# Optimization experiments

Measured on AMD Instinct MI355X. Metric: run time of the kernel, lower is better.

## Reference

```python
import jax, jax.numpy as jnp
import numpy as np

EPS_NORM = 1e-12  # F.normalize eps
EPS_LN = 1e-5     # nn.LayerNorm eps


def setup_inputs() -> dict:
    key = jax.random.key(0)
    ks = jax.random.split(key, 8)
    B, T, N, D = 16, 12, 300, 64
    feat = jax.random.normal(ks[0], (B, T, N, D), dtype=jnp.float32)
    weights = jax.random.uniform(ks[1], (D,), dtype=jnp.float32)
    sc = 1.0 / np.sqrt(D)
    w1 = jax.random.normal(ks[2], (D, D), dtype=jnp.float32) * sc
    b1 = jax.random.normal(ks[3], (D,), dtype=jnp.float32) * sc
    w2 = jax.random.normal(ks[4], (D, D), dtype=jnp.float32) * sc
    b2 = jax.random.normal(ks[5], (D,), dtype=jnp.float32) * sc
    gamma = jnp.ones((D,), dtype=jnp.float32)
    beta = jnp.zeros((D,), dtype=jnp.float32)
    return {"feat": feat, "weights": weights, "w1": w1, "b1": b1,
            "w2": w2, "b2": b2, "gamma": gamma, "beta": beta}


def _windows(x, T2):
    # x: [B,T,N,D] -> [B,T2,3N,D] where window i = concat(x[:,i], x[:,i+1], x[:,i+2]) over node dim
    B, T, N, D = x.shape
    w = jnp.stack([x[:, i:i + T2] for i in range(3)], axis=2)  # [B,T2,3,N,D]
    return w.reshape(B, T2, 3 * N, D)


def reference(feat, weights, w1, b1, w2, b2, gamma, beta):
    B, T, N, D = feat.shape
    T2 = T - 2
    # learned edge gating + L2-normalize along feature dim
    wf = feat * jax.nn.sigmoid(weights)
    nrm = jnp.sqrt(jnp.sum(wf * wf, axis=-1, keepdims=True))
    wf = wf / jnp.maximum(nrm, EPS_NORM)
    win = _windows(feat, T2)   # [B,T2,3N,D]
    wwin = _windows(wf, T2)    # [B,T2,3N,D]
    # learned adjacency: cosine-similarity gram matrix per window
    adj = jnp.einsum('btnd,btmd->btnm', wwin, wwin)  # [B,T2,3N,3N]
    # norm_adj: row normalization, zero rows stay zero
    deg = jnp.sum(adj, axis=-1, keepdims=True)
    dinv = jnp.where(deg == 0, 0.0, 1.0 / jnp.where(deg == 0, 1.0, deg))
    adj = adj * dinv
    # aggregate, keep last N rows (current timestep nodes)
    agg = jnp.einsum('btnm,btmd->btnd', adj, win)[:, :, -N:, :]  # [B,T2,N,D]
    # FFN (dropout is eval-mode identity): Linear -> ReLU -> Linear
    h = jnp.maximum(agg @ w1 + b1, 0.0) @ w2 + b2
    # residual + LayerNorm
    s = feat[:, 2:] + h
    mu = jnp.mean(s, axis=-1, keepdims=True)
    var = jnp.mean((s - mu) ** 2, axis=-1, keepdims=True)
    out = (s - mu) * jax.lax.rsqrt(var + EPS_LN) * gamma + beta
    return out  # [B, T-2, N, D]
```

## Files before the change

kernel.cpp:

```cpp
#include <hip/hip_runtime.h>
#include <math.h>

#define BB  16
#define TT  12
#define T2C 10
#define NN  300
#define DD  64
#define M3  900
#define NW  (BB*T2C)

typedef _Float16 f16;
typedef __attribute__((ext_vector_type(8)))  _Float16 f16x8;
typedef __attribute__((ext_vector_type(16))) float    f32x16;

#define KS 72

static __device__ inline unsigned pk2(f16 a, f16 b) {
    union { f16 h[2]; unsigned u; } x; x.h[0] = a; x.h[1] = b; return x.u;
}

__global__ __launch_bounds__(256) void k_pm(const float* __restrict__ feat,
                                            const float* __restrict__ weights,
                                            const float* __restrict__ w1,
                                            const float* __restrict__ w2,
                                            float* __restrict__ sigw,
                                            float* __restrict__ invn,
                                            float* __restrict__ tsum,
                                            f16* __restrict__ w1f,
                                            f16* __restrict__ w2f,
                                            float* __restrict__ Mt) {
    int blk = blockIdx.x;
    int tid = threadIdx.x;

    if (blk == BB * TT) {
        if (tid < 64) sigw[tid] = 1.0f / (1.0f + expf(-weights[tid]));
        for (int p = tid; p < 1024; p += 256) {
            int lane = p & 63, s = p >> 6;
            int mat = s >> 3, loc = s & 7, ct = loc >> 2, ks = loc & 3;
            int hcol = ct * 32 + (lane & 31);
            const float* w = mat ? w2 : w1;
            f16* dst = (mat ? w2f : w1f) + ((size_t)loc * 64 + lane) * 8;
            f16x8 v;
            #pragma unroll
            for (int j = 0; j < 8; j++) {
                int d = ks * 16 + 8 * (lane >> 5) + j;
                v[j] = (f16)w[d * DD + hcol];
            }
            *(f16x8*)dst = v;
        }
        return;
    }

    __shared__ f16 Kti[64 * KS];
    __shared__ f16 Vtt[64 * KS];
    __shared__ float sspart[64][8];
    __shared__ float invrow[64];
    __shared__ float tspp[32][64];

    int bt = blk;
    int row0 = bt * NN;
    int wv = tid >> 6, lane = tid & 63;
    int l31 = lane & 31, lh = lane >> 5;
    int ci = wv & 1, di = wv >> 1;
    int mr = (tid & 31) * 2;
    int cb = (tid >> 5) * 8;

    float sg[8];
    {
        float4 wv0 = *(const float4*)(weights + cb);
        float4 wv1 = *(const float4*)(weights + cb + 4);
        sg[0] = 1.f/(1.f+expf(-wv0.x)); sg[1] = 1.f/(1.f+expf(-wv0.y));
        sg[2] = 1.f/(1.f+expf(-wv0.z)); sg[3] = 1.f/(1.f+expf(-wv0.w));
        sg[4] = 1.f/(1.f+expf(-wv1.x)); sg[5] = 1.f/(1.f+expf(-wv1.y));
        sg[6] = 1.f/(1.f+expf(-wv1.z)); sg[7] = 1.f/(1.f+expf(-wv1.w));
    }

    float tacc[8];
    #pragma unroll
    for (int i = 0; i < 8; i++) tacc[i] = 0.f;
    f32x16 acc;
    #pragma unroll
    for (int i = 0; i < 16; i++) acc[i] = 0.f;

    for (int ep = 0; ep < 5; ep++) {
        __syncthreads();
        int gm0 = ep * 64 + mr, gm1 = gm0 + 1;
        bool ok0 = gm0 < NN, ok1 = gm1 < NN;
        int g0 = row0 + (ok0 ? gm0 : 0);
        int g1 = row0 + (ok1 ? gm1 : 0);
        float4 a0 = *(const float4*)(feat + (size_t)g0 * DD + cb);
        float4 a1 = *(const float4*)(feat + (size_t)g0 * DD + cb + 4);
        float4 b0 = *(const float4*)(feat + (size_t)g1 * DD + cb);
        float4 b1 = *(const float4*)(feat + (size_t)g1 * DD + cb + 4);
        float av[8] = {a0.x, a0.y, a0.z, a0.w, a1.x, a1.y, a1.z, a1.w};
        float bv[8] = {b0.x, b0.y, b0.z, b0.w, b1.x, b1.y, b1.z, b1.w};

        float ss0 = 0.f, ss1 = 0.f;
        #pragma unroll
        for (int i = 0; i < 8; i++) {
            float xa = av[i] * sg[i], xb = bv[i] * sg[i];
            ss0 += xa * xa; ss1 += xb * xb;
        }
        sspart[mr][tid >> 5] = ss0;
        sspart[mr + 1][tid >> 5] = ss1;
        __syncthreads();
        if (tid < 64) {
            float s = sspart[tid][0] + sspart[tid][1] + sspart[tid][2] + sspart[tid][3]
                    + sspart[tid][4] + sspart[tid][5] + sspart[tid][6] + sspart[tid][7];
            float in = 1.0f / fmaxf(sqrtf(s), 1e-12f);
            invrow[tid] = in;
            int grow = ep * 64 + tid;
            if (grow < NN) invn[row0 + grow] = in;
        }
        __syncthreads();
        float i0 = ok0 ? invrow[mr] : 0.f;
        float i1 = ok1 ? invrow[mr + 1] : 0.f;
        #pragma unroll
        for (int i = 0; i < 8; i++) {
            *(unsigned*)&Kti[(cb + i) * KS + mr] = pk2((f16)(av[i] * i0), (f16)(bv[i] * i1));
            *(unsigned*)&Vtt[(cb + i) * KS + mr] = pk2((f16)av[i], (f16)bv[i]);
            tacc[i] += av[i] * i0 + bv[i] * i1;
        }
        __syncthreads();
        #pragma unroll
        for (int ks = 0; ks < 4; ks++) {
            f16x8 af = *(const f16x8*)&Kti[(ci * 32 + l31) * KS + ks * 16 + 8 * lh];
            f16x8 bf = *(const f16x8*)&Vtt[(di * 32 + l31) * KS + ks * 16 + 8 * lh];
            acc = __builtin_amdgcn_mfma_f32_32x32x16_f16(af, bf, acc, 0, 0, 0);
        }
    }

    float* mb = Mt + (size_t)bt * 4096;
    #pragma unroll
    for (int g = 0; g < 4; g++)
        *(float4*)&mb[(di * 32 + l31) * 64 + ci * 32 + 8 * g + 4 * lh] =
            make_float4(acc[4 * g + 0], acc[4 * g + 1], acc[4 * g + 2], acc[4 * g + 3]);

    #pragma unroll
    for (int i = 0; i < 8; i++) tspp[tid & 31][cb + i] = tacc[i] * sg[i];
    __syncthreads();
    if (tid < 64) {
        float s = 0.f;
        #pragma unroll
        for (int g = 0; g < 32; g++) s += tspp[g][tid];
        tsum[(size_t)bt * 64 + tid] = s;
    }
}

__global__ __launch_bounds__(256) void k_U(const float* __restrict__ feat,
                                           const float* __restrict__ sigw,
                                           const float* __restrict__ invn,
                                           const float* __restrict__ tsum,
                                           const float* __restrict__ Mt,
                                           const f16* __restrict__ w1f,
                                           const f16* __restrict__ w2f,
                                           const float* __restrict__ b1,
                                           const float* __restrict__ b2,
                                           const float* __restrict__ gamma,
                                           const float* __restrict__ beta,
                                           float* __restrict__ out) {
    __shared__ union __align__(16) {
        f16 Mh[64 * KS];
        f16 Hl[64 * KS];
    } MH;
    __shared__ float Ol[64 * 68];
    __shared__ float red[64][4][2];
    __shared__ float rmax[64][4];
    __shared__ float scls[64];
    __shared__ float isls[64];
    __shared__ float degp[64][4];
    __shared__ float degs[64];
    __shared__ float ksumL[64];

    int blk = blockIdx.x;
    int wdw = blk % NW;
    int rb  = blk / NW;
    int t2 = wdw % T2C, b = wdw / T2C;
    int n0 = rb * 64;
    int qrow0 = (b * TT + t2 + 2) * NN;
    int tid = threadIdx.x;
    int wv = tid >> 6, lane = tid & 63;
    int l31 = lane & 31, lh = lane >> 5;
    int nt = wv & 1;
    int dt = wv >> 1;
    int ct = wv & 1, rt = wv >> 1;
    int r = tid >> 2, q = tid & 3, c0 = q * 16;

    f16x8 w1a[4], w2a[4];
    #pragma unroll
    for (int ks = 0; ks < 4; ks++) {
        w1a[ks] = *(const f16x8*)(w1f + ((size_t)(ct * 4 + ks) * 64 + lane) * 8);
        w2a[ks] = *(const f16x8*)(w2f + ((size_t)(ct * 4 + ks) * 64 + lane) * 8);
    }

    if (tid < 64) {
        const float* tp = tsum + (size_t)(b * TT + t2) * 64 + tid;
        ksumL[tid] = tp[0] + tp[64] + tp[128];
    }

    f16x8 qf[4];
    {
        int nloc = n0 + nt * 32 + l31;
        bool ok = nloc < NN;
        int gr = qrow0 + (ok ? nloc : 0);
        float in = ok ? invn[gr] : 0.f;
        #pragma unroll
        for (int ks = 0; ks < 4; ks++) {
            int cc = ks * 16 + 8 * lh;
            float4 f0 = *(const float4*)(feat + (size_t)gr * DD + cc);
            float4 f1 = *(const float4*)(feat + (size_t)gr * DD + cc + 4);
            float4 s0 = *(const float4*)(sigw + cc);
            float4 s1 = *(const float4*)(sigw + cc + 4);
            f16x8 qv;
            qv[0] = (f16)(f0.x * s0.x * s0.x * in); qv[1] = (f16)(f0.y * s0.y * s0.y * in);
            qv[2] = (f16)(f0.z * s0.z * s0.z * in); qv[3] = (f16)(f0.w * s0.w * s0.w * in);
            qv[4] = (f16)(f1.x * s1.x * s1.x * in); qv[5] = (f16)(f1.y * s1.y * s1.y * in);
            qv[6] = (f16)(f1.z * s1.z * s1.z * in); qv[7] = (f16)(f1.w * s1.w * s1.w * in);
            qf[ks] = qv;
        }
    }

    float ms[16];
    {
        const float* mtb = Mt + (size_t)(b * TT + t2) * 4096 + r * 64 + c0;
        #pragma unroll
        for (int i = 0; i < 4; i++) {
            float4 m0 = *(const float4*)(mtb + 4 * i);
            float4 m1 = *(const float4*)(mtb + 4096 + 4 * i);
            float4 m2 = *(const float4*)(mtb + 8192 + 4 * i);
            ms[4*i+0] = m0.x + m1.x + m2.x; ms[4*i+1] = m0.y + m1.y + m2.y;
            ms[4*i+2] = m0.z + m1.z + m2.z; ms[4*i+3] = m0.w + m1.w + m2.w;
        }
    }

    int n = n0 + r;
    int nc = (n < NN) ? n : (NN - 1);
    size_t frow = ((size_t)qrow0 + nc) * DD;
    float fv[16];
    #pragma unroll
    for (int i = 0; i < 4; i++) {
        float4 f = *(const float4*)(feat + frow + c0 + 4 * i);
        fv[4*i+0] = f.x; fv[4*i+1] = f.y; fv[4*i+2] = f.z; fv[4*i+3] = f.w;
    }
    float invq = invn[qrow0 + nc];

    __syncthreads();

    {
        float p = 0.f;
        #pragma unroll
        for (int i = 0; i < 4; i++) {
            float4 s = *(const float4*)(sigw + c0 + 4 * i);
            float4 k = *(const float4*)(ksumL + c0 + 4 * i);
            p += fv[4*i+0] * s.x * k.x + fv[4*i+1] * s.y * k.y
               + fv[4*i+2] * s.z * k.z + fv[4*i+3] * s.w * k.w;
        }
        degp[r][q] = p * invq;
    }

    #pragma unroll
    for (int hhalf = 0; hhalf < 2; hhalf++) {
        f16x8 v;
        #pragma unroll
        for (int j = 0; j < 8; j++) v[j] = (f16)ms[8 * hhalf + j];
        *(f16x8*)&MH.Mh[r * KS + c0 + 8 * hhalf] = v;
    }
    __syncthreads();

    if (tid < 64)
        degs[tid] = degp[tid][0] + degp[tid][1] + degp[tid][2] + degp[tid][3];

    f32x16 ua;
    #pragma unroll
    for (int i = 0; i < 16; i++) ua[i] = 0.f;
    #pragma unroll
    for (int ks = 0; ks < 4; ks++) {
        f16x8 af = *(const f16x8*)&MH.Mh[(dt * 32 + l31) * KS + ks * 16 + 8 * lh];
        ua = __builtin_amdgcn_mfma_f32_32x32x16_f16(af, qf[ks], ua, 0, 0, 0);
    }
    __syncthreads();

    {
        int nl = nt * 32 + l31;
        float dg = degs[nl];
        float dinv = (dg == 0.f) ? 0.f : 1.f / dg;
        #pragma unroll
        for (int g = 0; g < 4; g++)
            *(float4*)&Ol[nl * 68 + dt * 32 + 8 * g + 4 * lh] =
                make_float4(ua[4*g+0] * dinv, ua[4*g+1] * dinv,
                            ua[4*g+2] * dinv, ua[4*g+3] * dinv);
    }
    __syncthreads();

    {
        float mx = 0.f;
        #pragma unroll
        for (int i = 0; i < 16; i += 4) {
            float4 f = *(const float4*)&Ol[r * 68 + c0 + i];
            mx = fmaxf(mx, fmaxf(fmaxf(fabsf(f.x), fabsf(f.y)),
                                 fmaxf(fabsf(f.z), fabsf(f.w))));
        }
        rmax[r][q] = mx;
    }
    __syncthreads();
    if (q == 0) {
        float rm = fmaxf(fmaxf(rmax[r][0], rmax[r][1]),
                         fmaxf(rmax[r][2], rmax[r][3]));
        int e = 0;
        frexpf(rm, &e);
        scls[r] = (rm > 1.f) ? exp2f((float)-e) : 1.f;
        isls[r] = (rm > 1.f) ? exp2f((float)e) : 1.f;
    }
    __syncthreads();

    float sclrow = scls[rt * 32 + l31];
    f32x16 hc;
    #pragma unroll
    for (int i = 0; i < 16; i++) hc[i] = 0.f;
    #pragma unroll
    for (int ks = 0; ks < 4; ks++) {
        const float* prw = &Ol[(rt * 32 + l31) * 68 + ks * 16 + 8 * lh];
        float4 pa = *(const float4*)prw;
        float4 pb = *(const float4*)(prw + 4);
        f16x8 bf;
        bf[0] = (f16)(pa.x * sclrow); bf[1] = (f16)(pa.y * sclrow);
        bf[2] = (f16)(pa.z * sclrow); bf[3] = (f16)(pa.w * sclrow);
        bf[4] = (f16)(pb.x * sclrow); bf[5] = (f16)(pb.y * sclrow);
        bf[6] = (f16)(pb.z * sclrow); bf[7] = (f16)(pb.w * sclrow);
        hc = __builtin_amdgcn_mfma_f32_32x32x16_f16(w1a[ks], bf, hc, 0, 0, 0);
    }
    #pragma unroll
    for (int g = 0; g < 4; g++) {
        union { f16 h[4]; uint2 u; } p;
        #pragma unroll
        for (int i = 0; i < 4; i++) {
            int hcol = ct * 32 + 8 * g + 4 * lh + i;
            p.h[i] = (f16)fmaxf(hc[4 * g + i] + sclrow * b1[hcol], 0.f);
        }
        *(uint2*)&MH.Hl[(rt * 32 + l31) * KS + ct * 32 + 8 * g + 4 * lh] = p.u;
    }
    __syncthreads();

    f32x16 oc;
    #pragma unroll
    for (int i = 0; i < 16; i++) oc[i] = 0.f;
    #pragma unroll
    for (int ks = 0; ks < 4; ks++) {
        f16x8 bf = *(const f16x8*)&MH.Hl[(rt * 32 + l31) * KS + ks * 16 + 8 * lh];
        oc = __builtin_amdgcn_mfma_f32_32x32x16_f16(w2a[ks], bf, oc, 0, 0, 0);
    }
    __syncthreads();
    #pragma unroll
    for (int g = 0; g < 4; g++) {
        float4 o4 = make_float4(oc[4*g+0], oc[4*g+1], oc[4*g+2], oc[4*g+3]);
        *(float4*)&Ol[(rt * 32 + l31) * 68 + ct * 32 + 8 * g + 4 * lh] = o4;
    }
    __syncthreads();

    float is = isls[r];
    float v[16];
    float sum = 0.f;
    #pragma unroll
    for (int i = 0; i < 16; i++) {
        int c = c0 + i;
        float x = Ol[r * 68 + c] * is + b2[c] + fv[i];
        v[i] = x; sum += x;
    }
    red[r][q][0] = sum;
    __syncthreads();
    float mu = (red[r][0][0] + red[r][1][0] + red[r][2][0] + red[r][3][0]) * (1.f / 64.f);
    float s2 = 0.f;
    #pragma unroll
    for (int i = 0; i < 16; i++) { float d = v[i] - mu; s2 += d * d; }
    red[r][q][1] = s2;
    __syncthreads();
    float var = (red[r][0][1] + red[r][1][1] + red[r][2][1] + red[r][3][1]) * (1.f / 64.f);
    float rs = rsqrtf(var + 1e-5f);
    if (n < NN) {
        size_t grow = (size_t)wdw * NN + n;
        #pragma unroll
        for (int i4 = 0; i4 < 4; i4++) {
            int c = c0 + 4 * i4;
            float4 g4 = *(const float4*)(gamma + c);
            float4 be = *(const float4*)(beta + c);
            float4 o4;
            o4.x = (v[4*i4+0] - mu) * rs * g4.x + be.x;
            o4.y = (v[4*i4+1] - mu) * rs * g4.y + be.y;
            o4.z = (v[4*i4+2] - mu) * rs * g4.z + be.z;
            o4.w = (v[4*i4+3] - mu) * rs * g4.w + be.w;
            *(float4*)(out + grow * DD + c) = o4;
        }
    }
}

extern "C" void kernel_launch(void* const* d_in, const int* in_sizes, int n_in,
                              void* d_out, int out_size, void* d_ws, size_t ws_size,
                              hipStream_t stream) {
    const float* feat    = (const float*)d_in[0];
    const float* weights = (const float*)d_in[1];
    const float* w1      = (const float*)d_in[2];
    const float* b1      = (const float*)d_in[3];
    const float* w2      = (const float*)d_in[4];
    const float* b2      = (const float*)d_in[5];
    const float* gamma   = (const float*)d_in[6];
    const float* beta    = (const float*)d_in[7];
    float* out = (float*)d_out;

    float* sigw = (float*)d_ws;
    float* invn = sigw + 64;
    float* tsum = invn + BB * TT * NN;
    f16*   w1f  = (f16*)(tsum + BB * TT * DD);
    f16*   w2f  = w1f + 4096;
    float* Mt   = (float*)(w2f + 4096);

    k_pm<<<BB * TT + 1, 256, 0, stream>>>(feat, weights, w1, w2, sigw, invn,
                                          tsum, w1f, w2f, Mt);
    k_U<<<NW * 5, 256, 0, stream>>>(feat, sigw, invn, tsum, Mt, w1f, w2f,
                                    b1, b2, gamma, beta, out);
}
```

Before: 103.4 us.

## Fuse per-timestep prepass and per-window update into one kernel per window

Replaces the two-kernel scheme with a single kernel that runs one 512-thread block per window. Each block recomputes the 64x64 K^T V summary over all 900 window rows, splitting the reduction across two wave halves, and keeps the inverse norms and key sums in shared memory instead of going through global workspace. It then processes the five 64-row output tiles in two groups. This removes a launch and the global round-trip of the intermediates, and adds software prefetch of feat rows. In exchange, only 160 blocks are launched and each timestep's work is recomputed up to three times across overlapping windows.

```diff
diff --git a/kernel.cpp b/kernel.cpp
--- a/kernel.cpp
+++ b/kernel.cpp
@@ -6,64 +6,63 @@
 #define T2C 10
 #define NN  300
 #define DD  64
-#define M3  900
-#define NW  (BB*T2C)
+#define NWD (BB*T2C)
 
 typedef _Float16 f16;
 typedef __attribute__((ext_vector_type(8)))  _Float16 f16x8;
 typedef __attribute__((ext_vector_type(16))) float    f32x16;
 
-#define KS 72
+#define KSM 136
+#define KS  72
 
 static __device__ inline unsigned pk2(f16 a, f16 b) {
     union { f16 h[2]; unsigned u; } x; x.h[0] = a; x.h[1] = b; return x.u;
 }
 
-__global__ __launch_bounds__(256) void k_pm(const float* __restrict__ feat,
-                                            const float* __restrict__ weights,
-                                            const float* __restrict__ w1,
-                                            const float* __restrict__ w2,
-                                            float* __restrict__ sigw,
-                                            float* __restrict__ invn,
-                                            float* __restrict__ tsum,
-                                            f16* __restrict__ w1f,
-                                            f16* __restrict__ w2f,
-                                            float* __restrict__ Mt) {
+struct P1 {
+    f16 Kti[64 * KSM];
+    f16 Vtt[64 * KSM];
+    float sspart[128][8];
+    float invrow[128];
+};
+struct P2 {
+    float Ol[2][64 * 68];
+    f16   Hl[2][64 * KS];
+    float red[2][64][4][2];
+    float rmax[2][64][4];
+    float scls[2][64];
+    float isls[2][64];
+    float degp[2][64][4];
+    float degs[2][64];
+};
+
+__global__ __launch_bounds__(512, 2) void k_fused(
+        const float* __restrict__ feat,
+        const float* __restrict__ weights,
+        const float* __restrict__ w1,
+        const float* __restrict__ b1,
+        const float* __restrict__ w2,
+        const float* __restrict__ b2,
+        const float* __restrict__ gamma,
+        const float* __restrict__ beta,
+        float* __restrict__ out) {
+    __shared__ union __align__(16) { P1 p1; P2 p2; } SH;
+    __shared__ __align__(16) f16 Mh[64 * KS];
+    __shared__ __align__(16) float invq[NN + 4];
+    __shared__ __align__(16) float ksumL[64];
+    __shared__ __align__(16) float sigwL[64];
+
     int blk = blockIdx.x;
+    int wdw = (blk & 7) * (NWD / 8) + (blk >> 3);
+    int t2 = wdw % T2C, b = wdw / T2C;
     int tid = threadIdx.x;
-
-    if (blk == BB * TT) {
-        if (tid < 64) sigw[tid] = 1.0f / (1.0f + expf(-weights[tid]));
-        for (int p = tid; p < 1024; p += 256) {
-            int lane = p & 63, s = p >> 6;
-            int mat = s >> 3, loc = s & 7, ct = loc >> 2, ks = loc & 3;
-            int hcol = ct * 32 + (lane & 31);
-            const float* w = mat ? w2 : w1;
-            f16* dst = (mat ? w2f : w1f) + ((size_t)loc * 64 + lane) * 8;
-            f16x8 v;
-            #pragma unroll
-            for (int j = 0; j < 8; j++) {
-                int d = ks * 16 + 8 * (lane >> 5) + j;
-                v[j] = (f16)w[d * DD + hcol];
-            }
-            *(f16x8*)dst = v;
-        }
-        return;
-    }
-
-    __shared__ f16 Kti[64 * KS];
-    __shared__ f16 Vtt[64 * KS];
-    __shared__ float sspart[64][8];
-    __shared__ float invrow[64];
-    __shared__ float tspp[32][64];
-
-    int bt = blk;
-    int row0 = bt * NN;
-    int wv = tid >> 6, lane = tid & 63;
-    int l31 = lane & 31, lh = lane >> 5;
-    int ci = wv & 1, di = wv >> 1;
-    int mr = (tid & 31) * 2;
-    int cb = (tid >> 5) * 8;
+    int lane = tid & 63, l31 = lane & 31, lh = lane >> 5;
+    int wv = tid >> 6;
+    int ci = wv & 1, di = (wv >> 1) & 1, kh = wv >> 2;
+    int mr = (tid & 63) * 2;
+    int cb = (tid >> 6) * 8;
+
+    if (tid < 64) sigwL[tid] = 1.0f / (1.0f + expf(-weights[tid]));
 
     float sg[8];
     {
@@ -75,6 +74,8 @@
         sg[6] = 1.f/(1.f+expf(-wv1.z)); sg[7] = 1.f/(1.f+expf(-wv1.w));
     }
 
+    int baserow = (b * TT + t2) * NN;
+
     float tacc[8];
     #pragma unroll
     for (int i = 0; i < 8; i++) tacc[i] = 0.f;
@@ -82,313 +83,308 @@
     #pragma unroll
     for (int i = 0; i < 16; i++) acc[i] = 0.f;
 
-    for (int ep = 0; ep < 5; ep++) {
-        __syncthreads();
-        int gm0 = ep * 64 + mr, gm1 = gm0 + 1;
-        bool ok0 = gm0 < NN, ok1 = gm1 < NN;
-        int g0 = row0 + (ok0 ? gm0 : 0);
-        int g1 = row0 + (ok1 ? gm1 : 0);
-        float4 a0 = *(const float4*)(feat + (size_t)g0 * DD + cb);
-        float4 a1 = *(const float4*)(feat + (size_t)g0 * DD + cb + 4);
-        float4 b0 = *(const float4*)(feat + (size_t)g1 * DD + cb);
-        float4 b1 = *(const float4*)(feat + (size_t)g1 * DD + cb + 4);
-        float av[8] = {a0.x, a0.y, a0.z, a0.w, a1.x, a1.y, a1.z, a1.w};
-        float bv[8] = {b0.x, b0.y, b0.z, b0.w, b1.x, b1.y, b1.z, b1.w};
+#define LOADEP(EP, A, B) do { \
+        int M0_ = (EP) * 128 + mr; \
+        int g0_ = baserow + ((M0_ < 900) ? M0_ : 0); \
+        int g1_ = baserow + ((M0_ + 1 < 900) ? (M0_ + 1) : 0); \
+        float4 a0_ = *(const float4*)(feat + (size_t)g0_ * DD + cb); \
+        float4 a1_ = *(const float4*)(feat + (size_t)g0_ * DD + cb + 4); \
+        float4 b0_ = *(const float4*)(feat + (size_t)g1_ * DD + cb); \
+        float4 b1_ = *(const float4*)(feat + (size_t)g1_ * DD + cb + 4); \
+        A[0]=a0_.x; A[1]=a0_.y; A[2]=a0_.z; A[3]=a0_.w; \
+        A[4]=a1_.x; A[5]=a1_.y; A[6]=a1_.z; A[7]=a1_.w; \
+        B[0]=b0_.x; B[1]=b0_.y; B[2]=b0_.z; B[3]=b0_.w; \
+        B[4]=b1_.x; B[5]=b1_.y; B[6]=b1_.z; B[7]=b1_.w; \
+    } while (0)
+
+    float a_cur[8], b_cur[8];
+    LOADEP(0, a_cur, b_cur);
+
+    #pragma unroll
+    for (int ep = 0; ep < 8; ep++) {
+        int M0 = ep * 128 + mr;
+        bool ok0 = M0 < 900, ok1 = (M0 + 1) < 900;
 
         float ss0 = 0.f, ss1 = 0.f;
         #pragma unroll
         for (int i = 0; i < 8; i++) {
-            float xa = av[i] * sg[i], xb = bv[i] * sg[i];
+            float xa = a_cur[i] * sg[i], xb = b_cur[i] * sg[i];
             ss0 += xa * xa; ss1 += xb * xb;
         }
-        sspart[mr][tid >> 5] = ss0;
-        sspart[mr + 1][tid >> 5] = ss1;
-        __syncthreads();
-        if (tid < 64) {
-            float s = sspart[tid][0] + sspart[tid][1] + sspart[tid][2] + sspart[tid][3]
-                    + sspart[tid][4] + sspart[tid][5] + sspart[tid][6] + sspart[tid][7];
+        SH.p1.sspart[mr][wv] = ss0;
+        SH.p1.sspart[mr + 1][wv] = ss1;
+
+        float a_nxt[8], b_nxt[8];
+        if (ep < 7) LOADEP(ep + 1, a_nxt, b_nxt);
+
+        __syncthreads();
+        if (tid < 128) {
+            float s = SH.p1.sspart[tid][0] + SH.p1.sspart[tid][1]
+                    + SH.p1.sspart[tid][2] + SH.p1.sspart[tid][3]
+                    + SH.p1.sspart[tid][4] + SH.p1.sspart[tid][5]
+                    + SH.p1.sspart[tid][6] + SH.p1.sspart[tid][7];
             float in = 1.0f / fmaxf(sqrtf(s), 1e-12f);
-            invrow[tid] = in;
-            int grow = ep * 64 + tid;
-            if (grow < NN) invn[row0 + grow] = in;
-        }
-        __syncthreads();
-        float i0 = ok0 ? invrow[mr] : 0.f;
-        float i1 = ok1 ? invrow[mr + 1] : 0.f;
+            SH.p1.invrow[tid] = in;
+            int M = ep * 128 + tid;
+            if (M >= 600 && M < 900) invq[M - 600] = in;
+        }
+        __syncthreads();
+        float i0 = ok0 ? SH.p1.invrow[mr] : 0.f;
+        float i1 = ok1 ? SH.p1.invrow[mr + 1] : 0.f;
         #pragma unroll
         for (int i = 0; i < 8; i++) {
-            *(unsigned*)&Kti[(cb + i) * KS + mr] = pk2((f16)(av[i] * i0), (f16)(bv[i] * i1));
-            *(unsigned*)&Vtt[(cb + i) * KS + mr] = pk2((f16)av[i], (f16)bv[i]);
-            tacc[i] += av[i] * i0 + bv[i] * i1;
+            *(unsigned*)&SH.p1.Kti[(cb + i) * KSM + mr] =
+                pk2((f16)(a_cur[i] * i0), (f16)(b_cur[i] * i1));
+            *(unsigned*)&SH.p1.Vtt[(cb + i) * KSM + mr] =
+                pk2((f16)a_cur[i], (f16)b_cur[i]);
+            tacc[i] += a_cur[i] * i0 + b_cur[i] * i1;
         }
         __syncthreads();
         #pragma unroll
         for (int ks = 0; ks < 4; ks++) {
-            f16x8 af = *(const f16x8*)&Kti[(ci * 32 + l31) * KS + ks * 16 + 8 * lh];
-            f16x8 bf = *(const f16x8*)&Vtt[(di * 32 + l31) * KS + ks * 16 + 8 * lh];
+            f16x8 af = *(const f16x8*)&SH.p1.Kti[(ci*32+l31)*KSM + kh*64 + ks*16 + 8*lh];
+            f16x8 bf = *(const f16x8*)&SH.p1.Vtt[(di*32+l31)*KSM + kh*64 + ks*16 + 8*lh];
             acc = __builtin_amdgcn_mfma_f32_32x32x16_f16(af, bf, acc, 0, 0, 0);
         }
-    }
-
-    float* mb = Mt + (size_t)bt * 4096;
+        if (ep < 7) {
+            #pragma unroll
+            for (int i = 0; i < 8; i++) { a_cur[i] = a_nxt[i]; b_cur[i] = b_nxt[i]; }
+        }
+    }
+#undef LOADEP
+
+    __syncthreads();
+    float* Mw   = (float*)SH.p1.Kti;
+    float* tspp = (float*)SH.p1.Vtt;
+    if (kh == 1) {
+        #pragma unroll
+        for (int g4 = 0; g4 < 4; g4++)
+            *(float4*)&Mw[(di*32+l31)*68 + ci*32 + 8*g4 + 4*lh] =
+                make_float4(acc[4*g4+0], acc[4*g4+1], acc[4*g4+2], acc[4*g4+3]);
+    }
     #pragma unroll
-    for (int g = 0; g < 4; g++)
-        *(float4*)&mb[(di * 32 + l31) * 64 + ci * 32 + 8 * g + 4 * lh] =
-            make_float4(acc[4 * g + 0], acc[4 * g + 1], acc[4 * g + 2], acc[4 * g + 3]);
-
-    #pragma unroll
-    for (int i = 0; i < 8; i++) tspp[tid & 31][cb + i] = tacc[i] * sg[i];
+    for (int i = 0; i < 8; i++) tspp[(tid & 63) * 64 + cb + i] = tacc[i] * sg[i];
     __syncthreads();
+    if (kh == 0) {
+        #pragma unroll
+        for (int g4 = 0; g4 < 4; g4++) {
+            float4 m = *(const float4*)&Mw[(di*32+l31)*68 + ci*32 + 8*g4 + 4*lh];
+            union { f16 h[4]; uint2 u; } p;
+            p.h[0] = (f16)(acc[4*g4+0] + m.x);
+            p.h[1] = (f16)(acc[4*g4+1] + m.y);
+            p.h[2] = (f16)(acc[4*g4+2] + m.z);
+            p.h[3] = (f16)(acc[4*g4+3] + m.w);
+            *(uint2*)&Mh[(di*32+l31)*KS + ci*32 + 8*g4 + 4*lh] = p.u;
+        }
+    }
     if (tid < 64) {
         float s = 0.f;
-        #pragma unroll
-        for (int g = 0; g < 32; g++) s += tspp[g][tid];
-        tsum[(size_t)bt * 64 + tid] = s;
-    }
-}
-
-__global__ __launch_bounds__(256) void k_U(const float* __restrict__ feat,
-                                           const float* __restrict__ sigw,
-                                           const float* __restrict__ invn,
-                                           const float* __restrict__ tsum,
-                                           const float* __restrict__ Mt,
-                                           const f16* __restrict__ w1f,
-                                           const f16* __restrict__ w2f,
-                                           const float* __restrict__ b1,
-                                           const float* __restrict__ b2,
-                                           const float* __restrict__ gamma,
-                                           const float* __restrict__ beta,
-                                           float* __restrict__ out) {
-    __shared__ union __align__(16) {
-        f16 Mh[64 * KS];
-        f16 Hl[64 * KS];
-    } MH;
-    __shared__ float Ol[64 * 68];
-    __shared__ float red[64][4][2];
-    __shared__ float rmax[64][4];
-    __shared__ float scls[64];
-    __shared__ float isls[64];
-    __shared__ float degp[64][4];
-    __shared__ float degs[64];
-    __shared__ float ksumL[64];
-
-    int blk = blockIdx.x;
-    int wdw = blk % NW;
-    int rb  = blk / NW;
-    int t2 = wdw % T2C, b = wdw / T2C;
-    int n0 = rb * 64;
+        #pragma unroll 8
+        for (int j = 0; j < 64; j++) s += tspp[j * 64 + tid];
+        ksumL[tid] = s;
+    }
+    __syncthreads();
+
+    int grp = tid >> 8;
+    int ltid = tid & 255;
+    int wv_l = ltid >> 6;
+    int nt = wv_l & 1, dt = wv_l >> 1;
+    int ct = wv_l & 1, rt = wv_l >> 1;
+    int r = ltid >> 2, q = ltid & 3, c0 = q * 16;
     int qrow0 = (b * TT + t2 + 2) * NN;
-    int tid = threadIdx.x;
-    int wv = tid >> 6, lane = tid & 63;
-    int l31 = lane & 31, lh = lane >> 5;
-    int nt = wv & 1;
-    int dt = wv >> 1;
-    int ct = wv & 1, rt = wv >> 1;
-    int r = tid >> 2, q = tid & 3, c0 = q * 16;
 
     f16x8 w1a[4], w2a[4];
     #pragma unroll
     for (int ks = 0; ks < 4; ks++) {
-        w1a[ks] = *(const f16x8*)(w1f + ((size_t)(ct * 4 + ks) * 64 + lane) * 8);
-        w2a[ks] = *(const f16x8*)(w2f + ((size_t)(ct * 4 + ks) * 64 + lane) * 8);
-    }
-
-    if (tid < 64) {
-        const float* tp = tsum + (size_t)(b * TT + t2) * 64 + tid;
-        ksumL[tid] = tp[0] + tp[64] + tp[128];
-    }
-
-    f16x8 qf[4];
-    {
-        int nloc = n0 + nt * 32 + l31;
-        bool ok = nloc < NN;
-        int gr = qrow0 + (ok ? nloc : 0);
-        float in = ok ? invn[gr] : 0.f;
+        f16x8 v1, v2;
+        #pragma unroll
+        for (int j = 0; j < 8; j++) {
+            int drow = ks * 16 + 8 * lh + j;
+            int hcol = ct * 32 + l31;
+            v1[j] = (f16)w1[drow * DD + hcol];
+            v2[j] = (f16)w2[drow * DD + hcol];
+        }
+        w1a[ks] = v1; w2a[ks] = v2;
+    }
+
+    for (int it = 0; it < 3; it++) {
+        int tile = it * 2 + grp;
+        bool act = tile < 5;
+        int n0 = tile * 64;
+
+        __syncthreads();
+
+        f16x8 qf[4];
+        {
+            int nloc = n0 + nt * 32 + l31;
+            bool ok = act && (nloc < NN);
+            int ni = ok ? nloc : 0;
+            int gr = qrow0 + ni;
+            float in = ok ? invq[ni] : 0.f;
+            #pragma unroll
+            for (int ks = 0; ks < 4; ks++) {
+                int cc = ks * 16 + 8 * lh;
+                float4 f0 = *(const float4*)(feat + (size_t)gr * DD + cc);
+                float4 f1 = *(const float4*)(feat + (size_t)gr * DD + cc + 4);
+                float4 s0 = *(const float4*)&sigwL[cc];
+                float4 s1 = *(const float4*)&sigwL[cc + 4];
+                f16x8 qv;
+                qv[0] = (f16)(f0.x*s0.x*s0.x*in); qv[1] = (f16)(f0.y*s0.y*s0.y*in);
+                qv[2] = (f16)(f0.z*s0.z*s0.z*in); qv[3] = (f16)(f0.w*s0.w*s0.w*in);
+                qv[4] = (f16)(f1.x*s1.x*s1.x*in); qv[5] = (f16)(f1.y*s1.y*s1.y*in);
+                qv[6] = (f16)(f1.z*s1.z*s1.z*in); qv[7] = (f16)(f1.w*s1.w*s1.w*in);
+                qf[ks] = qv;
+            }
+        }
+
+        int n = n0 + r;
+        int nc = (n < NN) ? n : (NN - 1);
+        size_t frow = ((size_t)qrow0 + nc) * DD;
+        float fv[16];
+        #pragma unroll
+        for (int i = 0; i < 4; i++) {
+            float4 f = *(const float4*)(feat + frow + c0 + 4 * i);
+            fv[4*i+0] = f.x; fv[4*i+1] = f.y; fv[4*i+2] = f.z; fv[4*i+3] = f.w;
+        }
+        float invqr = invq[nc];
+
+        {
+            float p = 0.f;
+            #pragma unroll
+            for (int i = 0; i < 4; i++) {
+                float4 s = *(const float4*)&sigwL[c0 + 4 * i];
+                float4 k = *(const float4*)&ksumL[c0 + 4 * i];
+                p += fv[4*i+0]*s.x*k.x + fv[4*i+1]*s.y*k.y
+                   + fv[4*i+2]*s.z*k.z + fv[4*i+3]*s.w*k.w;
+            }
+            SH.p2.degp[grp][r][q] = p * invqr;
+        }
+
+        f32x16 ua;
+        #pragma unroll
+        for (int i = 0; i < 16; i++) ua[i] = 0.f;
         #pragma unroll
         for (int ks = 0; ks < 4; ks++) {
-            int cc = ks * 16 + 8 * lh;
-            float4 f0 = *(const float4*)(feat + (size_t)gr * DD + cc);
-            float4 f1 = *(const float4*)(feat + (size_t)gr * DD + cc + 4);
-            float4 s0 = *(const float4*)(sigw + cc);
-            float4 s1 = *(const float4*)(sigw + cc + 4);
-            f16x8 qv;
-            qv[0] = (f16)(f0.x * s0.x * s0.x * in); qv[1] = (f16)(f0.y * s0.y * s0.y * in);
-            qv[2] = (f16)(f0.z * s0.z * s0.z * in); qv[3] = (f16)(f0.w * s0.w * s0.w * in);
-            qv[4] = (f16)(f1.x * s1.x * s1.x * in); qv[5] = (f16)(f1.y * s1.y * s1.y * in);
-            qv[6] = (f16)(f1.z * s1.z * s1.z * in); qv[7] = (f16)(f1.w * s1.w * s1.w * in);
-            qf[ks] = qv;
-        }
-    }
-
-    float ms[16];
-    {
-        const float* mtb = Mt + (size_t)(b * TT + t2) * 4096 + r * 64 + c0;
-        #pragma unroll
-        for (int i = 0; i < 4; i++) {
-            float4 m0 = *(const float4*)(mtb + 4 * i);
-            float4 m1 = *(const float4*)(mtb + 4096 + 4 * i);
-            float4 m2 = *(const float4*)(mtb + 8192 + 4 * i);
-            ms[4*i+0] = m0.x + m1.x + m2.x; ms[4*i+1] = m0.y + m1.y + m2.y;
-            ms[4*i+2] = m0.z + m1.z + m2.z; ms[4*i+3] = m0.w + m1.w + m2.w;
-        }
-    }
-
-    int n = n0 + r;
-    int nc = (n < NN) ? n : (NN - 1);
-    size_t frow = ((size_t)qrow0 + nc) * DD;
-    float fv[16];
-    #pragma unroll
-    for (int i = 0; i < 4; i++) {
-        float4 f = *(const float4*)(feat + frow + c0 + 4 * i);
-        fv[4*i+0] = f.x; fv[4*i+1] = f.y; fv[4*i+2] = f.z; fv[4*i+3] = f.w;
-    }
-    float invq = invn[qrow0 + nc];
-
-    __syncthreads();
-
-    {
-        float p = 0.f;
-        #pragma unroll
-        for (int i = 0; i < 4; i++) {
-            float4 s = *(const float4*)(sigw + c0 + 4 * i);
-            float4 k = *(const float4*)(ksumL + c0 + 4 * i);
-            p += fv[4*i+0] * s.x * k.x + fv[4*i+1] * s.y * k.y
-               + fv[4*i+2] * s.z * k.z + fv[4*i+3] * s.w * k.w;
-        }
-        degp[r][q] = p * invq;
-    }
-
-    #pragma unroll
-    for (int hhalf = 0; hhalf < 2; hhalf++) {
-        f16x8 v;
-        #pragma unroll
-        for (int j = 0; j < 8; j++) v[j] = (f16)ms[8 * hhalf + j];
-        *(f16x8*)&MH.Mh[r * KS + c0 + 8 * hhalf] = v;
-    }
-    __syncthreads();
-
-    if (tid < 64)
-        degs[tid] = degp[tid][0] + degp[tid][1] + degp[tid][2] + degp[tid][3];
-
-    f32x16 ua;
-    #pragma unroll
-    for (int i = 0; i < 16; i++) ua[i] = 0.f;
-    #pragma unroll
-    for (int ks = 0; ks < 4; ks++) {
-        f16x8 af = *(const f16x8*)&MH.Mh[(dt * 32 + l31) * KS + ks * 16 + 8 * lh];
-        ua = __builtin_amdgcn_mfma_f32_32x32x16_f16(af, qf[ks], ua, 0, 0, 0);
-    }
-    __syncthreads();
-
-    {
-        int nl = nt * 32 + l31;
-        float dg = degs[nl];
-        float dinv = (dg == 0.f) ? 0.f : 1.f / dg;
-        #pragma unroll
-        for (int g = 0; g < 4; g++)
-            *(float4*)&Ol[nl * 68 + dt * 32 + 8 * g + 4 * lh] =
-                make_float4(ua[4*g+0] * dinv, ua[4*g+1] * dinv,
-                            ua[4*g+2] * dinv, ua[4*g+3] * dinv);
-    }
-    __syncthreads();
-
-    {
-        float mx = 0.f;
-        #pragma unroll
-        for (int i = 0; i < 16; i += 4) {
-            float4 f = *(const float4*)&Ol[r * 68 + c0 + i];
-            mx = fmaxf(mx, fmaxf(fmaxf(fabsf(f.x), fabsf(f.y)),
-                                 fmaxf(fabsf(f.z), fabsf(f.w))));
-        }
-        rmax[r][q] = mx;
-    }
-    __syncthreads();
-    if (q == 0) {
-        float rm = fmaxf(fmaxf(rmax[r][0], rmax[r][1]),
-                         fmaxf(rmax[r][2], rmax[r][3]));
-        int e = 0;
-        frexpf(rm, &e);
-        scls[r] = (rm > 1.f) ? exp2f((float)-e) : 1.f;
-        isls[r] = (rm > 1.f) ? exp2f((float)e) : 1.f;
-    }
-    __syncthreads();
-
-    float sclrow = scls[rt * 32 + l31];
-    f32x16 hc;
-    #pragma unroll
-    for (int i = 0; i < 16; i++) hc[i] = 0.f;
-    #pragma unroll
-    for (int ks = 0; ks < 4; ks++) {
-        const float* prw = &Ol[(rt * 32 + l31) * 68 + ks * 16 + 8 * lh];
-        float4 pa = *(const float4*)prw;
-        float4 pb = *(const float4*)(prw + 4);
-        f16x8 bf;
-        bf[0] = (f16)(pa.x * sclrow); bf[1] = (f16)(pa.y * sclrow);
-        bf[2] = (f16)(pa.z * sclrow); bf[3] = (f16)(pa.w * sclrow);
-        bf[4] = (f16)(pb.x * sclrow); bf[5] = (f16)(pb.y * sclrow);
-        bf[6] = (f16)(pb.z * sclrow); bf[7] = (f16)(pb.w * sclrow);
-        hc = __builtin_amdgcn_mfma_f32_32x32x16_f16(w1a[ks], bf, hc, 0, 0, 0);
-    }
-    #pragma unroll
-    for (int g = 0; g < 4; g++) {
-        union { f16 h[4]; uint2 u; } p;
-        #pragma unroll
-        for (int i = 0; i < 4; i++) {
-            int hcol = ct * 32 + 8 * g + 4 * lh + i;
-            p.h[i] = (f16)fmaxf(hc[4 * g + i] + sclrow * b1[hcol], 0.f);
-        }
-        *(uint2*)&MH.Hl[(rt * 32 + l31) * KS + ct * 32 + 8 * g + 4 * lh] = p.u;
-    }
-    __syncthreads();
-
-    f32x16 oc;
-    #pragma unroll
-    for (int i = 0; i < 16; i++) oc[i] = 0.f;
-    #pragma unroll
-    for (int ks = 0; ks < 4; ks++) {
-        f16x8 bf = *(const f16x8*)&MH.Hl[(rt * 32 + l31) * KS + ks * 16 + 8 * lh];
-        oc = __builtin_amdgcn_mfma_f32_32x32x16_f16(w2a[ks], bf, oc, 0, 0, 0);
-    }
-    __syncthreads();
-    #pragma unroll
-    for (int g = 0; g < 4; g++) {
-        float4 o4 = make_float4(oc[4*g+0], oc[4*g+1], oc[4*g+2], oc[4*g+3]);
-        *(float4*)&Ol[(rt * 32 + l31) * 68 + ct * 32 + 8 * g + 4 * lh] = o4;
-    }
-    __syncthreads();
-
-    float is = isls[r];
-    float v[16];
-    float sum = 0.f;
-    #pragma unroll
-    for (int i = 0; i < 16; i++) {
-        int c = c0 + i;
-        float x = Ol[r * 68 + c] * is + b2[c] + fv[i];
-        v[i] = x; sum += x;
-    }
-    red[r][q][0] = sum;
-    __syncthreads();
-    float mu = (red[r][0][0] + red[r][1][0] + red[r][2][0] + red[r][3][0]) * (1.f / 64.f);
-    float s2 = 0.f;
-    #pragma unroll
-    for (int i = 0; i < 16; i++) { float d = v[i] - mu; s2 += d * d; }
-    red[r][q][1] = s2;
-    __syncthreads();
-    float var = (red[r][0][1] + red[r][1][1] + red[r][2][1] + red[r][3][1]) * (1.f / 64.f);
-    float rs = rsqrtf(var + 1e-5f);
-    if (n < NN) {
-        size_t grow = (size_t)wdw * NN + n;
-        #pragma unroll
-        for (int i4 = 0; i4 < 4; i4++) {
-            int c = c0 + 4 * i4;
-            float4 g4 = *(const float4*)(gamma + c);
-            float4 be = *(const float4*)(beta + c);
-            float4 o4;
-            o4.x = (v[4*i4+0] - mu) * rs * g4.x + be.x;
-            o4.y = (v[4*i4+1] - mu) * rs * g4.y + be.y;
-            o4.z = (v[4*i4+2] - mu) * rs * g4.z + be.z;
-            o4.w = (v[4*i4+3] - mu) * rs * g4.w + be.w;
-            *(float4*)(out + grow * DD + c) = o4;
+            f16x8 af = *(const f16x8*)&Mh[(dt*32+l31)*KS + ks*16 + 8*lh];
+            ua = __builtin_amdgcn_mfma_f32_32x32x16_f16(af, qf[ks], ua, 0, 0, 0);
+        }
+        __syncthreads();
+        if (ltid < 64)
+            SH.p2.degs[grp][ltid] = SH.p2.degp[grp][ltid][0] + SH.p2.degp[grp][ltid][1]
+                                  + SH.p2.degp[grp][ltid][2] + SH.p2.degp[grp][ltid][3];
+        __syncthreads();
+
+        {
+            int nl = nt * 32 + l31;
+            float dg = SH.p2.degs[grp][nl];
+            float dinv = (dg == 0.f) ? 0.f : 1.f / dg;
+            #pragma unroll
+            for (int g4 = 0; g4 < 4; g4++)
+                *(float4*)&SH.p2.Ol[grp][nl * 68 + dt * 32 + 8 * g4 + 4 * lh] =
+                    make_float4(ua[4*g4+0]*dinv, ua[4*g4+1]*dinv,
+                                ua[4*g4+2]*dinv, ua[4*g4+3]*dinv);
+        }
+        __syncthreads();
+
+        {
+            float mx = 0.f;
+            #pragma unroll
+            for (int i = 0; i < 16; i += 4) {
+                float4 f = *(const float4*)&SH.p2.Ol[grp][r * 68 + c0 + i];
+                mx = fmaxf(mx, fmaxf(fmaxf(fabsf(f.x), fabsf(f.y)),
+                                     fmaxf(fabsf(f.z), fabsf(f.w))));
+            }
+            SH.p2.rmax[grp][r][q] = mx;
+        }
+        __syncthreads();
+        if (q == 0) {
+            float rm = fmaxf(fmaxf(SH.p2.rmax[grp][r][0], SH.p2.rmax[grp][r][1]),
+                             fmaxf(SH.p2.rmax[grp][r][2], SH.p2.rmax[grp][r][3]));
+            int e = 0;
+            frexpf(rm, &e);
+            SH.p2.scls[grp][r] = (rm > 1.f) ? exp2f((float)-e) : 1.f;
+            SH.p2.isls[grp][r] = (rm > 1.f) ? exp2f((float)e) : 1.f;
+        }
+        __syncthreads();
+
+        float sclrow = SH.p2.scls[grp][rt * 32 + l31];
+        f32x16 hc;
+        #pragma unroll
+        for (int i = 0; i < 16; i++) hc[i] = 0.f;
+        #pragma unroll
+        for (int ks = 0; ks < 4; ks++) {
+            const float* prw = &SH.p2.Ol[grp][(rt*32+l31)*68 + ks*16 + 8*lh];
+            float4 pa = *(const float4*)prw;
+            float4 pb = *(const float4*)(prw + 4);
+            f16x8 bf;
+            bf[0] = (f16)(pa.x * sclrow); bf[1] = (f16)(pa.y * sclrow);
+            bf[2] = (f16)(pa.z * sclrow); bf[3] = (f16)(pa.w * sclrow);
+            bf[4] = (f16)(pb.x * sclrow); bf[5] = (f16)(pb.y * sclrow);
+            bf[6] = (f16)(pb.z * sclrow); bf[7] = (f16)(pb.w * sclrow);
+            hc = __builtin_amdgcn_mfma_f32_32x32x16_f16(w1a[ks], bf, hc, 0, 0, 0);
+        }
+        #pragma unroll
+        for (int g4 = 0; g4 < 4; g4++) {
+            union { f16 h[4]; uint2 u; } p;
+            #pragma unroll
+            for (int i = 0; i < 4; i++) {
+                int hcol = ct * 32 + 8 * g4 + 4 * lh + i;
+                p.h[i] = (f16)fmaxf(hc[4 * g4 + i] + sclrow * b1[hcol], 0.f);
+            }
+            *(uint2*)&SH.p2.Hl[grp][(rt*32+l31)*KS + ct*32 + 8*g4 + 4*lh] = p.u;
+        }
+        __syncthreads();
+
+        f32x16 oc;
+        #pragma unroll
+        for (int i = 0; i < 16; i++) oc[i] = 0.f;
+        #pragma unroll
+        for (int ks = 0; ks < 4; ks++) {
+            f16x8 bf = *(const f16x8*)&SH.p2.Hl[grp][(rt*32+l31)*KS + ks*16 + 8*lh];
+            oc = __builtin_amdgcn_mfma_f32_32x32x16_f16(w2a[ks], bf, oc, 0, 0, 0);
+        }
+        __syncthreads();
+        #pragma unroll
+        for (int g4 = 0; g4 < 4; g4++)
+            *(float4*)&SH.p2.Ol[grp][(rt*32+l31)*68 + ct*32 + 8*g4 + 4*lh] =
+                make_float4(oc[4*g4+0], oc[4*g4+1], oc[4*g4+2], oc[4*g4+3]);
+        __syncthreads();
+
+        float is = SH.p2.isls[grp][r];
+        float v[16];
+        float sum = 0.f;
+        #pragma unroll
+        for (int i = 0; i < 16; i++) {
+            int c = c0 + i;
+            float x = SH.p2.Ol[grp][r * 68 + c] * is + b2[c] + fv[i];
+            v[i] = x; sum += x;
+        }
+        SH.p2.red[grp][r][q][0] = sum;
+        __syncthreads();
+        float mu = (SH.p2.red[grp][r][0][0] + SH.p2.red[grp][r][1][0]
+                  + SH.p2.red[grp][r][2][0] + SH.p2.red[grp][r][3][0]) * (1.f / 64.f);
+        float s2 = 0.f;
+        #pragma unroll
+        for (int i = 0; i < 16; i++) { float d = v[i] - mu; s2 += d * d; }
+        SH.p2.red[grp][r][q][1] = s2;
+        __syncthreads();
+        float var = (SH.p2.red[grp][r][0][1] + SH.p2.red[grp][r][1][1]
+                   + SH.p2.red[grp][r][2][1] + SH.p2.red[grp][r][3][1]) * (1.f / 64.f);
+        float rs = rsqrtf(var + 1e-5f);
+        if (act && n < NN) {
+            size_t grow = (size_t)wdw * NN + n;
+            #pragma unroll
+            for (int i4 = 0; i4 < 4; i4++) {
+                int c = c0 + 4 * i4;
+                float4 g4v = *(const float4*)(gamma + c);
+                float4 be  = *(const float4*)(beta + c);
+                float4 o4;
+                o4.x = (v[4*i4+0] - mu) * rs * g4v.x + be.x;
+                o4.y = (v[4*i4+1] - mu) * rs * g4v.y + be.y;
+                o4.z = (v[4*i4+2] - mu) * rs * g4v.z + be.z;
+                o4.w = (v[4*i4+3] - mu) * rs * g4v.w + be.w;
+                *(float4*)(out + grow * DD + c) = o4;
+            }
         }
     }
 }
@@ -404,17 +400,8 @@
     const float* b2      = (const float*)d_in[5];
     const float* gamma   = (const float*)d_in[6];
     const float* beta    = (const float*)d_in[7];
-    float* out = (float*)d_out;
-
-    float* sigw = (float*)d_ws;
-    float* invn = sigw + 64;
-    float* tsum = invn + BB * TT * NN;
-    f16*   w1f  = (f16*)(tsum + BB * TT * DD);
-    f16*   w2f  = w1f + 4096;
-    float* Mt   = (float*)(w2f + 4096);
-
-    k_pm<<<BB * TT + 1, 256, 0, stream>>>(feat, weights, w1, w2, sigw, invn,
-                                          tsum, w1f, w2f, Mt);
-    k_U<<<NW * 5, 256, 0, stream>>>(feat, sigw, invn, tsum, Mt, w1f, w2f,
-                                    b1, b2, gamma, beta, out);
+    (void)in_sizes; (void)n_in; (void)out_size; (void)d_ws; (void)ws_size;
+
+    k_fused<<<NWD, 512, 0, stream>>>(feat, weights, w1, b1, w2, b2, gamma, beta,
+                                     (float*)d_out);
 }
```

New measurement: 110.9 us. 1.07x slower.

## Widen k_pm to 512 threads, split-K MFMA across waves, prefetch next epoch

Applied to the files above, without the earlier changes.

The per-timestep precompute kernel now runs 512 threads per block and processes 128 rows per epoch (3 epochs instead of 5). The K dimension of the MFMA is split across two wave halves, and the two partial results are reduced through shared memory. Feature loads for the next epoch are issued before the barriers so their latency overlaps the norm reduction. This aims to cut per-block latency in a grid of only 193 blocks, at the cost of more shared memory, registers and an extra reduction step.

```diff
diff --git a/kernel.cpp b/kernel.cpp
--- a/kernel.cpp
+++ b/kernel.cpp
@@ -13,13 +13,14 @@
 typedef __attribute__((ext_vector_type(8)))  _Float16 f16x8;
 typedef __attribute__((ext_vector_type(16))) float    f32x16;
 
-#define KS 72
+#define KS  72
+#define KSM 136
 
 static __device__ inline unsigned pk2(f16 a, f16 b) {
     union { f16 h[2]; unsigned u; } x; x.h[0] = a; x.h[1] = b; return x.u;
 }
 
-__global__ __launch_bounds__(256) void k_pm(const float* __restrict__ feat,
+__global__ __launch_bounds__(512) void k_pm(const float* __restrict__ feat,
                                             const float* __restrict__ weights,
                                             const float* __restrict__ w1,
                                             const float* __restrict__ w2,
@@ -34,16 +35,16 @@
 
     if (blk == BB * TT) {
         if (tid < 64) sigw[tid] = 1.0f / (1.0f + expf(-weights[tid]));
-        for (int p = tid; p < 1024; p += 256) {
+        for (int p = tid; p < 1024; p += 512) {
             int lane = p & 63, s = p >> 6;
-            int mat = s >> 3, loc = s & 7, ct = loc >> 2, ks = loc & 3;
+            int mat = s >> 3, loc = s & 7, ct = loc >> 2, ksv = loc & 3;
             int hcol = ct * 32 + (lane & 31);
             const float* w = mat ? w2 : w1;
             f16* dst = (mat ? w2f : w1f) + ((size_t)loc * 64 + lane) * 8;
             f16x8 v;
             #pragma unroll
             for (int j = 0; j < 8; j++) {
-                int d = ks * 16 + 8 * (lane >> 5) + j;
+                int d = ksv * 16 + 8 * (lane >> 5) + j;
                 v[j] = (f16)w[d * DD + hcol];
             }
             *(f16x8*)dst = v;
@@ -51,19 +52,20 @@
         return;
     }
 
-    __shared__ f16 Kti[64 * KS];
-    __shared__ f16 Vtt[64 * KS];
-    __shared__ float sspart[64][8];
-    __shared__ float invrow[64];
-    __shared__ float tspp[32][64];
+    __shared__ union __align__(16) {
+        struct { f16 Kti[64 * KSM]; f16 Vtt[64 * KSM]; } s;
+        struct { float Mw[64 * 68]; float tspp[64 * 64]; } r;
+    } SH;
+    __shared__ float sspart[128][8];
+    __shared__ float invrow[128];
 
     int bt = blk;
     int row0 = bt * NN;
     int wv = tid >> 6, lane = tid & 63;
     int l31 = lane & 31, lh = lane >> 5;
-    int ci = wv & 1, di = wv >> 1;
-    int mr = (tid & 31) * 2;
-    int cb = (tid >> 5) * 8;
+    int ci = wv & 1, di = (wv >> 1) & 1, kh = wv >> 2;
+    int mr = (tid & 63) * 2;
+    int cb = (tid >> 6) * 8;
 
     float sg[8];
     {
@@ -82,34 +84,47 @@
     #pragma unroll
     for (int i = 0; i < 16; i++) acc[i] = 0.f;
 
-    for (int ep = 0; ep < 5; ep++) {
+#define LOADEP(EP, A, B) do { \
+        int M0_ = (EP) * 128 + mr; \
+        int g0_ = row0 + ((M0_ < NN) ? M0_ : 0); \
+        int g1_ = row0 + ((M0_ + 1 < NN) ? (M0_ + 1) : 0); \
+        float4 a0_ = *(const float4*)(feat + (size_t)g0_ * DD + cb); \
+        float4 a1_ = *(const float4*)(feat + (size_t)g0_ * DD + cb + 4); \
+        float4 b0_ = *(const float4*)(feat + (size_t)g1_ * DD + cb); \
+        float4 b1_ = *(const float4*)(feat + (size_t)g1_ * DD + cb + 4); \
+        A[0]=a0_.x; A[1]=a0_.y; A[2]=a0_.z; A[3]=a0_.w; \
+        A[4]=a1_.x; A[5]=a1_.y; A[6]=a1_.z; A[7]=a1_.w; \
+        B[0]=b0_.x; B[1]=b0_.y; B[2]=b0_.z; B[3]=b0_.w; \
+        B[4]=b1_.x; B[5]=b1_.y; B[6]=b1_.z; B[7]=b1_.w; \
+    } while (0)
+
+    float a_cur[8], b_cur[8];
+    LOADEP(0, a_cur, b_cur);
+
+    #pragma unroll
+    for (int ep = 0; ep < 3; ep++) {
+        int M0 = ep * 128 + mr;
+        bool ok0 = M0 < NN, ok1 = (M0 + 1) < NN;
+
+        float ss0 = 0.f, ss1 = 0.f;
+        #pragma unroll
+        for (int i = 0; i < 8; i++) {
+            float xa = a_cur[i] * sg[i], xb = b_cur[i] * sg[i];
+            ss0 += xa * xa; ss1 += xb * xb;
+        }
+        sspart[mr][wv] = ss0;
+        sspart[mr + 1][wv] = ss1;
+
+        float a_nxt[8], b_nxt[8];
+        if (ep < 2) LOADEP(ep + 1, a_nxt, b_nxt);
+
         __syncthreads();
-        int gm0 = ep * 64 + mr, gm1 = gm0 + 1;
-        bool ok0 = gm0 < NN, ok1 = gm1 < NN;
-        int g0 = row0 + (ok0 ? gm0 : 0);
-        int g1 = row0 + (ok1 ? gm1 : 0);
-        float4 a0 = *(const float4*)(feat + (size_t)g0 * DD + cb);
-        float4 a1 = *(const float4*)(feat + (size_t)g0 * DD + cb + 4);
-        float4 b0 = *(const float4*)(feat + (size_t)g1 * DD + cb);
-        float4 b1 = *(const float4*)(feat + (size_t)g1 * DD + cb + 4);
-        float av[8] = {a0.x, a0.y, a0.z, a0.w, a1.x, a1.y, a1.z, a1.w};
-        float bv[8] = {b0.x, b0.y, b0.z, b0.w, b1.x, b1.y, b1.z, b1.w};
-
-        float ss0 = 0.f, ss1 = 0.f;
-        #pragma unroll
-        for (int i = 0; i < 8; i++) {
-            float xa = av[i] * sg[i], xb = bv[i] * sg[i];
-            ss0 += xa * xa; ss1 += xb * xb;
-        }
-        sspart[mr][tid >> 5] = ss0;
-        sspart[mr + 1][tid >> 5] = ss1;
-        __syncthreads();
-        if (tid < 64) {
+        if (tid < 128) {
             float s = sspart[tid][0] + sspart[tid][1] + sspart[tid][2] + sspart[tid][3]
                     + sspart[tid][4] + sspart[tid][5] + sspart[tid][6] + sspart[tid][7];
             float in = 1.0f / fmaxf(sqrtf(s), 1e-12f);
             invrow[tid] = in;
-            int grow = ep * 64 + tid;
+            int grow = ep * 128 + tid;
             if (grow < NN) invn[row0 + grow] = in;
         }
         __syncthreads();
@@ -117,32 +132,50 @@
         float i1 = ok1 ? invrow[mr + 1] : 0.f;
         #pragma unroll
         for (int i = 0; i < 8; i++) {
-            *(unsigned*)&Kti[(cb + i) * KS + mr] = pk2((f16)(av[i] * i0), (f16)(bv[i] * i1));
-            *(unsigned*)&Vtt[(cb + i) * KS + mr] = pk2((f16)av[i], (f16)bv[i]);
-            tacc[i] += av[i] * i0 + bv[i] * i1;
+            *(unsigned*)&SH.s.Kti[(cb + i) * KSM + mr] =
+                pk2((f16)(a_cur[i] * i0), (f16)(b_cur[i] * i1));
+            *(unsigned*)&SH.s.Vtt[(cb + i) * KSM + mr] =
+                pk2((f16)a_cur[i], (f16)b_cur[i]);
+            tacc[i] += a_cur[i] * i0 + b_cur[i] * i1;
         }
         __syncthreads();
         #pragma unroll
         for (int ks = 0; ks < 4; ks++) {
-            f16x8 af = *(const f16x8*)&Kti[(ci * 32 + l31) * KS + ks * 16 + 8 * lh];
-            f16x8 bf = *(const f16x8*)&Vtt[(di * 32 + l31) * KS + ks * 16 + 8 * lh];
+            f16x8 af = *(const f16x8*)&SH.s.Kti[(ci*32+l31)*KSM + kh*64 + ks*16 + 8*lh];
+            f16x8 bf = *(const f16x8*)&SH.s.Vtt[(di*32+l31)*KSM + kh*64 + ks*16 + 8*lh];
             acc = __builtin_amdgcn_mfma_f32_32x32x16_f16(af, bf, acc, 0, 0, 0);
         }
-    }
-
-    float* mb = Mt + (size_t)bt * 4096;
-    #pragma unroll
-    for (int g = 0; g < 4; g++)
-        *(float4*)&mb[(di * 32 + l31) * 64 + ci * 32 + 8 * g + 4 * lh] =
-            make_float4(acc[4 * g + 0], acc[4 * g + 1], acc[4 * g + 2], acc[4 * g + 3]);
-
-    #pragma unroll
-    for (int i = 0; i < 8; i++) tspp[tid & 31][cb + i] = tacc[i] * sg[i];
-    __syncthreads();
+        if (ep < 2) {
+            #pragma unroll
+            for (int i = 0; i < 8; i++) { a_cur[i] = a_nxt[i]; b_cur[i] = b_nxt[i]; }
+        }
+    }
+#undef LOADEP
+
+    __syncthreads();
+    if (kh == 1) {
+        #pragma unroll
+        for (int g = 0; g < 4; g++)
+            *(float4*)&SH.r.Mw[(di*32+l31)*68 + ci*32 + 8*g + 4*lh] =
+                make_float4(acc[4*g+0], acc[4*g+1], acc[4*g+2], acc[4*g+3]);
+    }
+    #pragma unroll
+    for (int i = 0; i < 8; i++) SH.r.tspp[(tid & 63) * 64 + cb + i] = tacc[i] * sg[i];
+    __syncthreads();
+    if (kh == 0) {
+        float* mb = Mt + (size_t)bt * 4096;
+        #pragma unroll
+        for (int g = 0; g < 4; g++) {
+            float4 m = *(const float4*)&SH.r.Mw[(di*32+l31)*68 + ci*32 + 8*g + 4*lh];
+            *(float4*)&mb[(di * 32 + l31) * 64 + ci * 32 + 8 * g + 4 * lh] =
+                make_float4(acc[4*g+0] + m.x, acc[4*g+1] + m.y,
+                            acc[4*g+2] + m.z, acc[4*g+3] + m.w);
+        }
+    }
     if (tid < 64) {
         float s = 0.f;
-        #pragma unroll
-        for (int g = 0; g < 32; g++) s += tspp[g][tid];
+        #pragma unroll 8
+        for (int j = 0; j < 64; j++) s += SH.r.tspp[j * 64 + tid];
         tsum[(size_t)bt * 64 + tid] = s;
     }
 }
@@ -413,7 +446,7 @@
     f16*   w2f  = w1f + 4096;
     float* Mt   = (float*)(w2f + 4096);
 
-    k_pm<<<BB * TT + 1, 256, 0, stream>>>(feat, weights, w1, w2, sigw, invn,
+    k_pm<<<BB * TT + 1, 512, 0, stream>>>(feat, weights, w1, w2, sigw, invn,
                                           tsum, w1f, w2f, Mt);
     k_U<<<NW * 5, 256, 0, stream>>>(feat, sigw, invn, tsum, Mt, w1f, w2f,
                                     b1, b2, gamma, beta, out);
```

Result: no change. 102.0 us (-1.3%).
